# Kernel optimization log

Measured on AMD Instinct MI355X. Metric: run time of the kernel, lower is better.

The kernel has to match this reference:

```python
import jax, jax.numpy as jnp
import numpy as np


def setup_inputs() -> dict:
    key = jax.random.key(0)
    ks = jax.random.split(key, 8)
    B, S, D, H = 32, 8192, 256, 256  # batch, seq_len, input_dim, hidden_dim
    bound = 1.0 / np.sqrt(H)
    x = jax.random.normal(ks[0], (B, H), dtype=jnp.float32)
    context = jax.random.normal(ks[1], (B, S, D), dtype=jnp.float32)
    mask = jax.random.randint(ks[2], (B, S), 0, 2, dtype=jnp.int32)
    # input_linear: Linear(H, H)
    W_in = jax.random.uniform(ks[3], (H, H), jnp.float32, -bound, bound)
    b_in = jax.random.uniform(ks[4], (H,), jnp.float32, -bound, bound)
    # context_linear: Conv1d(D, H, kernel=1) == pointwise linear over features
    W_ctx = jax.random.uniform(ks[5], (H, D), jnp.float32, -1.0 / np.sqrt(D), 1.0 / np.sqrt(D))
    b_ctx = jax.random.uniform(ks[6], (H,), jnp.float32, -1.0 / np.sqrt(D), 1.0 / np.sqrt(D))
    V = jax.random.uniform(ks[7], (H,), jnp.float32, -bound, bound)
    return {"x": x, "context": context, "mask": mask,
            "W_in": W_in, "b_in": b_in, "W_ctx": W_ctx, "b_ctx": b_ctx, "V": V}


def reference(x, context, mask, W_in, b_in, W_ctx, b_ctx, V):
    # inp: [B, H] -> broadcast over seq as [B, 1, H]
    inp = (x @ W_in.T + b_in)[:, None, :]
    # ctx: Conv1d(kernel=1) over permuted context == per-position linear: [B, S, H]
    ctx = jnp.einsum('bsd,hd->bsh', context, W_ctx) + b_ctx
    # score: V . tanh(inp + ctx) reduced over H -> [B, S]
    att = jnp.einsum('bsh,h->bs', jnp.tanh(inp + ctx), V)
    att = 10.0 * jnp.tanh(att)
    att = jnp.where(mask.astype(bool), att, -jnp.inf)
    ans = jax.nn.softmax(att, axis=1)
    indices = jnp.argmax(ans, axis=1)
    p = jnp.max(ans, axis=1)
    return (indices, p[:, None], mask.astype(bool))
```

## Files before the change

kernel.cpp:

```cpp
#include <hip/hip_runtime.h>
#include <math.h>

#define S_LEN 8192
#define BATCH 32
#define HDIM 256
#define DDIM 256
#define SCHUNK 512
#define NSUB 8
#define TSUB 64
#define LDK 264

typedef float f32x4 __attribute__((ext_vector_type(4)));
typedef __fp16 h16x2 __attribute__((ext_vector_type(2)));
typedef __fp16 h16x4 __attribute__((ext_vector_type(4)));
typedef _Float16 f16x8 __attribute__((ext_vector_type(8)));

static __device__ __forceinline__ float fast_tanh(float x) {
    float e = __expf(2.0f * x);
    return 1.0f - 2.0f / (e + 1.0f);
}

static __device__ __forceinline__ void cvt_store(f32x4 v, _Float16* ph, _Float16* pl) {
    h16x2 h0 = __builtin_amdgcn_cvt_pkrtz(v[0], v[1]);
    h16x2 h1 = __builtin_amdgcn_cvt_pkrtz(v[2], v[3]);
    h16x2 l0 = __builtin_amdgcn_cvt_pkrtz(v[0] - (float)h0[0], v[1] - (float)h0[1]);
    h16x2 l1 = __builtin_amdgcn_cvt_pkrtz(v[2] - (float)h1[0], v[3] - (float)h1[1]);
    h16x4 hi; hi[0] = h0[0]; hi[1] = h0[1]; hi[2] = h1[0]; hi[3] = h1[1];
    h16x4 lo; lo[0] = l0[0]; lo[1] = l0[1]; lo[2] = l1[0]; lo[3] = l1[1];
    *(h16x4*)ph = hi;
    *(h16x4*)pl = lo;
}

__global__ void prep_kernel(const float* __restrict__ x,
                            const float* __restrict__ W_in,
                            const float* __restrict__ b_in,
                            const float* __restrict__ W_ctx,
                            const float* __restrict__ b_ctx,
                            float* __restrict__ cin,
                            _Float16* __restrict__ Wf) {
    __shared__ float xs[DDIM];
    const int bx = blockIdx.x;
    const int t  = threadIdx.x;
    if (bx < BATCH) {
        xs[t] = x[bx * DDIM + t];
        __syncthreads();
        const float* wr = W_in + t * DDIM;
        float acc = b_in[t] + b_ctx[t];
        #pragma unroll 8
        for (int d = 0; d < DDIM; ++d) acc += xs[d] * wr[d];
        cin[bx * HDIM + t] = acc;
    } else {
        const int g  = (bx - BATCH) * 256 + t;
        const int ht = g >> 9;
        const int ks = (g >> 6) & 7;
        const int l  = g & 63;
        const int h  = ht * 16 + (l & 15);
        const int d0 = ks * 32 + (l >> 4) * 8;
        const float* src = W_ctx + h * DDIM + d0;
        f16x8 vh;
        #pragma unroll
        for (int j = 0; j < 8; ++j) vh[j] = (_Float16)src[j];
        *(f16x8*)(Wf + (size_t)g * 8) = vh;
    }
}

__launch_bounds__(1024, 4)
__global__ void att_kernel(const float* __restrict__ context,
                           const int* __restrict__ mask,
                           const float* __restrict__ cin,
                           const float* __restrict__ V,
                           const _Float16* __restrict__ Wf,
                           float* __restrict__ att,
                           float* __restrict__ out_mask) {
    __shared__ __align__(16) _Float16 a_hi[2][TSUB * LDK];
    __shared__ __align__(16) _Float16 a_lo[2][TSUB * LDK];
    __shared__ float att_part[2][16][TSUB];

    const int schunk = blockIdx.x;
    const int b      = blockIdx.y;
    const int t      = threadIdx.x;
    const int w      = t >> 6;
    const int l      = t & 63;
    const int lane16 = l & 15;
    const int q      = l >> 4;

    f16x8 wfrag[8];
    #pragma unroll
    for (int ks = 0; ks < 8; ++ks)
        wfrag[ks] = *(const f16x8*)(Wf + (size_t)((w * 8 + ks) * 64 + l) * 8);

    float cinr[4], vr[4];
    #pragma unroll
    for (int r = 0; r < 4; ++r) {
        int h = w * 16 + q * 4 + r;
        cinr[r] = cin[b * HDIM + h];
        vr[r]   = V[h];
    }

    const float* cbase = context + ((size_t)b * S_LEN + (size_t)schunk * SCHUNK) * DDIM;

    #pragma unroll
    for (int i = 0; i < 4; ++i) {
        int f = i * 1024 + t, row = f >> 6, c4 = f & 63;
        f32x4 v = *(const f32x4*)(cbase + row * DDIM + c4 * 4);
        cvt_store(v, &a_hi[0][row * LDK + c4 * 4], &a_lo[0][row * LDK + c4 * 4]);
    }
    __syncthreads();

    for (int it = 0; it < NSUB; ++it) {
        const int cur = it & 1;
        const bool pre = (it + 1 < NSUB);

        f32x4 pf[4];
        if (pre) {
            const float* nb = cbase + (size_t)(it + 1) * TSUB * DDIM;
            #pragma unroll
            for (int i = 0; i < 4; ++i) {
                int f = i * 1024 + t, row = f >> 6, c4 = f & 63;
                pf[i] = *(const f32x4*)(nb + row * DDIM + c4 * 4);
            }
        }

        f32x4 acc[4];
        #pragma unroll
        for (int nt = 0; nt < 4; ++nt) acc[nt] = (f32x4){0.f, 0.f, 0.f, 0.f};
        #pragma unroll
        for (int ks = 0; ks < 8; ++ks) {
            #pragma unroll
            for (int nt = 0; nt < 4; ++nt) {
                int o = (nt * 16 + lane16) * LDK + ks * 32 + q * 8;
                f16x8 bh = *(const f16x8*)(&a_hi[cur][o]);
                f16x8 bl = *(const f16x8*)(&a_lo[cur][o]);
                acc[nt] = __builtin_amdgcn_mfma_f32_16x16x32_f16(wfrag[ks], bh, acc[nt], 0, 0, 0);
                acc[nt] = __builtin_amdgcn_mfma_f32_16x16x32_f16(wfrag[ks], bl, acc[nt], 0, 0, 0);
            }
        }

        #pragma unroll
        for (int nt = 0; nt < 4; ++nt) {
            float p = 0.f;
            #pragma unroll
            for (int r = 0; r < 4; ++r)
                p += fast_tanh(acc[nt][r] + cinr[r]) * vr[r];
            p += __shfl_xor(p, 16);
            p += __shfl_xor(p, 32);
            if (l < 16) att_part[cur][w][nt * 16 + l] = p;
        }

        if (pre) {
            #pragma unroll
            for (int i = 0; i < 4; ++i) {
                int f = i * 1024 + t, row = f >> 6, c4 = f & 63;
                cvt_store(pf[i], &a_hi[cur ^ 1][row * LDK + c4 * 4],
                                 &a_lo[cur ^ 1][row * LDK + c4 * 4]);
            }
        }
        __syncthreads();

        if (t < TSUB) {
            float a = 0.f;
            #pragma unroll
            for (int ww = 0; ww < 16; ++ww) a += att_part[cur][ww][t];
            a = 10.0f * fast_tanh(a);
            int s  = schunk * SCHUNK + it * TSUB + t;
            int mk = mask[b * S_LEN + s];
            att[(size_t)b * S_LEN + s]      = mk ? a : -INFINITY;
            out_mask[(size_t)b * S_LEN + s] = mk ? 1.0f : 0.0f;
        }
    }
}

__global__ void reduce_kernel(const float* __restrict__ att,
                              float* __restrict__ out) {
    __shared__ float smax[256];
    __shared__ int   sidx[256];
    const int b = blockIdx.x;
    const int t = threadIdx.x;
    const float* row = att + (size_t)b * S_LEN;

    float best = -INFINITY;
    int   bid  = 0x7fffffff;
    for (int s = t; s < S_LEN; s += 256) {
        float v = row[s];
        if (v > best) { best = v; bid = s; }
    }
    smax[t] = best; sidx[t] = bid;
    __syncthreads();
    for (int off = 128; off > 0; off >>= 1) {
        if (t < off) {
            float ov = smax[t + off]; int oi = sidx[t + off];
            if (ov > smax[t] || (ov == smax[t] && oi < sidx[t])) { smax[t] = ov; sidx[t] = oi; }
        }
        __syncthreads();
    }
    const float mx = smax[0];
    const int   ix = sidx[0];
    __syncthreads();

    float sum = 0.f;
    for (int s = t; s < S_LEN; s += 256)
        sum += __expf(row[s] - mx);
    smax[t] = sum;
    __syncthreads();
    for (int off = 128; off > 0; off >>= 1) {
        if (t < off) smax[t] += smax[t + off];
        __syncthreads();
    }
    if (t == 0) {
        out[b]         = (float)ix;
        out[BATCH + b] = 1.0f / smax[0];
    }
}

extern "C" void kernel_launch(void* const* d_in, const int* in_sizes, int n_in,
                              void* d_out, int out_size, void* d_ws, size_t ws_size,
                              hipStream_t stream) {
    const float* x       = (const float*)d_in[0];
    const float* context = (const float*)d_in[1];
    const int*   mask    = (const int*)d_in[2];
    const float* W_in    = (const float*)d_in[3];
    const float* b_in    = (const float*)d_in[4];
    const float* W_ctx   = (const float*)d_in[5];
    const float* b_ctx   = (const float*)d_in[6];
    const float* V       = (const float*)d_in[7];
    float* out = (float*)d_out;

    char* ws = (char*)d_ws;
    float*    cin = (float*)ws;
    _Float16* Wf  = (_Float16*)(ws + 32 * 1024);
    float*    att = (float*)(ws + 160 * 1024);

    float* out_mask = out + 64;

    prep_kernel<<<64, 256, 0, stream>>>(x, W_in, b_in, W_ctx, b_ctx, cin, Wf);
    dim3 grid(S_LEN / SCHUNK, BATCH);
    att_kernel<<<grid, 1024, 0, stream>>>(context, mask, cin, V, Wf, att, out_mask);
    reduce_kernel<<<BATCH, 256, 0, stream>>>(att, out);
}
```

Baseline: 416.5 us.

## Give each wave two H-tiles to reuse B fragments, halve block size

The attention kernel now runs 8 waves of 512 threads, each covering two 16-row H tiles. Each LDS load of context fragments therefore feeds twice as many MFMAs, which halves LDS read traffic per MFMA. The accumulators are initialised with the bias vector, so the per-element add before tanh goes away. The sequence chunk doubles to halve the grid, and the reduce kernel uses 1024 threads. In exchange, register pressure per thread rises (16 weight fragments, 8 accumulators, 8 prefetch vectors) and there are fewer blocks, which may reduce occupancy and latency hiding for this memory-bound stream.

```diff
diff --git a/kernel.cpp b/kernel.cpp
--- a/kernel.cpp
+++ b/kernel.cpp
@@ -5,8 +5,8 @@
 #define BATCH 32
 #define HDIM 256
 #define DDIM 256
-#define SCHUNK 512
-#define NSUB 8
+#define SCHUNK 1024
+#define NSUB 16
 #define TSUB 64
 #define LDK 264
 
@@ -64,7 +64,7 @@
     }
 }
 
-__launch_bounds__(1024, 4)
+__launch_bounds__(512, 2)
 __global__ void att_kernel(const float* __restrict__ context,
                            const int* __restrict__ mask,
                            const float* __restrict__ cin,
@@ -74,7 +74,7 @@
                            float* __restrict__ out_mask) {
     __shared__ __align__(16) _Float16 a_hi[2][TSUB * LDK];
     __shared__ __align__(16) _Float16 a_lo[2][TSUB * LDK];
-    __shared__ float att_part[2][16][TSUB];
+    __shared__ float att_part[2][8][TSUB];
 
     const int schunk = blockIdx.x;
     const int b      = blockIdx.y;
@@ -84,24 +84,28 @@
     const int lane16 = l & 15;
     const int q      = l >> 4;
 
-    f16x8 wfrag[8];
+    f16x8 wfrag[2][8];
     #pragma unroll
-    for (int ks = 0; ks < 8; ++ks)
-        wfrag[ks] = *(const f16x8*)(Wf + (size_t)((w * 8 + ks) * 64 + l) * 8);
-
-    float cinr[4], vr[4];
+    for (int ht = 0; ht < 2; ++ht)
+        #pragma unroll
+        for (int ks = 0; ks < 8; ++ks)
+            wfrag[ht][ks] = *(const f16x8*)(Wf + (size_t)(((w * 2 + ht) * 8 + ks) * 64 + l) * 8);
+
+    f32x4 cinr4[2], vr4[2];
     #pragma unroll
-    for (int r = 0; r < 4; ++r) {
-        int h = w * 16 + q * 4 + r;
-        cinr[r] = cin[b * HDIM + h];
-        vr[r]   = V[h];
-    }
+    for (int ht = 0; ht < 2; ++ht)
+        #pragma unroll
+        for (int r = 0; r < 4; ++r) {
+            int h = (w * 2 + ht) * 16 + q * 4 + r;
+            cinr4[ht][r] = cin[b * HDIM + h];
+            vr4[ht][r]   = V[h];
+        }
 
     const float* cbase = context + ((size_t)b * S_LEN + (size_t)schunk * SCHUNK) * DDIM;
 
     #pragma unroll
-    for (int i = 0; i < 4; ++i) {
-        int f = i * 1024 + t, row = f >> 6, c4 = f & 63;
+    for (int i = 0; i < 8; ++i) {
+        int f = i * 512 + t, row = f >> 6, c4 = f & 63;
         f32x4 v = *(const f32x4*)(cbase + row * DDIM + c4 * 4);
         cvt_store(v, &a_hi[0][row * LDK + c4 * 4], &a_lo[0][row * LDK + c4 * 4]);
     }
@@ -111,19 +115,21 @@
         const int cur = it & 1;
         const bool pre = (it + 1 < NSUB);
 
-        f32x4 pf[4];
+        f32x4 pf[8];
         if (pre) {
             const float* nb = cbase + (size_t)(it + 1) * TSUB * DDIM;
             #pragma unroll
-            for (int i = 0; i < 4; ++i) {
-                int f = i * 1024 + t, row = f >> 6, c4 = f & 63;
+            for (int i = 0; i < 8; ++i) {
+                int f = i * 512 + t, row = f >> 6, c4 = f & 63;
                 pf[i] = *(const f32x4*)(nb + row * DDIM + c4 * 4);
             }
         }
 
-        f32x4 acc[4];
-        #pragma unroll
-        for (int nt = 0; nt < 4; ++nt) acc[nt] = (f32x4){0.f, 0.f, 0.f, 0.f};
+        f32x4 acc[2][4];
+        #pragma unroll
+        for (int ht = 0; ht < 2; ++ht)
+            #pragma unroll
+            for (int nt = 0; nt < 4; ++nt) acc[ht][nt] = cinr4[ht];
         #pragma unroll
         for (int ks = 0; ks < 8; ++ks) {
             #pragma unroll
@@ -131,8 +137,11 @@
                 int o = (nt * 16 + lane16) * LDK + ks * 32 + q * 8;
                 f16x8 bh = *(const f16x8*)(&a_hi[cur][o]);
                 f16x8 bl = *(const f16x8*)(&a_lo[cur][o]);
-                acc[nt] = __builtin_amdgcn_mfma_f32_16x16x32_f16(wfrag[ks], bh, acc[nt], 0, 0, 0);
-                acc[nt] = __builtin_amdgcn_mfma_f32_16x16x32_f16(wfrag[ks], bl, acc[nt], 0, 0, 0);
+                #pragma unroll
+                for (int ht = 0; ht < 2; ++ht) {
+                    acc[ht][nt] = __builtin_amdgcn_mfma_f32_16x16x32_f16(wfrag[ht][ks], bh, acc[ht][nt], 0, 0, 0);
+                    acc[ht][nt] = __builtin_amdgcn_mfma_f32_16x16x32_f16(wfrag[ht][ks], bl, acc[ht][nt], 0, 0, 0);
+                }
             }
         }
 
@@ -140,8 +149,10 @@
         for (int nt = 0; nt < 4; ++nt) {
             float p = 0.f;
             #pragma unroll
-            for (int r = 0; r < 4; ++r)
-                p += fast_tanh(acc[nt][r] + cinr[r]) * vr[r];
+            for (int ht = 0; ht < 2; ++ht)
+                #pragma unroll
+                for (int r = 0; r < 4; ++r)
+                    p += fast_tanh(acc[ht][nt][r]) * vr4[ht][r];
             p += __shfl_xor(p, 16);
             p += __shfl_xor(p, 32);
             if (l < 16) att_part[cur][w][nt * 16 + l] = p;
@@ -149,8 +160,8 @@
 
         if (pre) {
             #pragma unroll
-            for (int i = 0; i < 4; ++i) {
-                int f = i * 1024 + t, row = f >> 6, c4 = f & 63;
+            for (int i = 0; i < 8; ++i) {
+                int f = i * 512 + t, row = f >> 6, c4 = f & 63;
                 cvt_store(pf[i], &a_hi[cur ^ 1][row * LDK + c4 * 4],
                                  &a_lo[cur ^ 1][row * LDK + c4 * 4]);
             }
@@ -160,7 +171,7 @@
         if (t < TSUB) {
             float a = 0.f;
             #pragma unroll
-            for (int ww = 0; ww < 16; ++ww) a += att_part[cur][ww][t];
+            for (int ww = 0; ww < 8; ++ww) a += att_part[cur][ww][t];
             a = 10.0f * fast_tanh(a);
             int s  = schunk * SCHUNK + it * TSUB + t;
             int mk = mask[b * S_LEN + s];
@@ -172,21 +183,21 @@
 
 __global__ void reduce_kernel(const float* __restrict__ att,
                               float* __restrict__ out) {
-    __shared__ float smax[256];
-    __shared__ int   sidx[256];
+    __shared__ float smax[1024];
+    __shared__ int   sidx[1024];
     const int b = blockIdx.x;
     const int t = threadIdx.x;
     const float* row = att + (size_t)b * S_LEN;
 
     float best = -INFINITY;
     int   bid  = 0x7fffffff;
-    for (int s = t; s < S_LEN; s += 256) {
+    for (int s = t; s < S_LEN; s += 1024) {
         float v = row[s];
         if (v > best) { best = v; bid = s; }
     }
     smax[t] = best; sidx[t] = bid;
     __syncthreads();
-    for (int off = 128; off > 0; off >>= 1) {
+    for (int off = 512; off > 0; off >>= 1) {
         if (t < off) {
             float ov = smax[t + off]; int oi = sidx[t + off];
             if (ov > smax[t] || (ov == smax[t] && oi < sidx[t])) { smax[t] = ov; sidx[t] = oi; }
@@ -198,11 +209,11 @@
     __syncthreads();
 
     float sum = 0.f;
-    for (int s = t; s < S_LEN; s += 256)
+    for (int s = t; s < S_LEN; s += 1024)
         sum += __expf(row[s] - mx);
     smax[t] = sum;
     __syncthreads();
-    for (int off = 128; off > 0; off >>= 1) {
+    for (int off = 512; off > 0; off >>= 1) {
         if (t < off) smax[t] += smax[t + off];
         __syncthreads();
     }
@@ -234,6 +245,6 @@
 
     prep_kernel<<<64, 256, 0, stream>>>(x, W_in, b_in, W_ctx, b_ctx, cin, Wf);
     dim3 grid(S_LEN / SCHUNK, BATCH);
-    att_kernel<<<grid, 1024, 0, stream>>>(context, mask, cin, V, Wf, att, out_mask);
-    reduce_kernel<<<BATCH, 256, 0, stream>>>(att, out);
-}
+    att_kernel<<<grid, 512, 0, stream>>>(context, mask, cin, V, Wf, att, out_mask);
+    reduce_kernel<<<BATCH, 1024, 0, stream>>>(att, out);
+}
```

Measured after the change: 400.7 us. 3.8% less time.
